# Performance work log

Hardware: AMD Instinct MI355X
Metric: run time of the kernel (lower is better)

Reference implementation:

```python
import jax, jax.numpy as jnp
import numpy as np

N = 100_000   # num destination nodes (adj rows)
M = 100_000   # num source/neighbor nodes (adj cols)
E = 3_200_000 # num edges (avg degree 32)
D_IN = 128
DIM = 128
LEAKY_ALPHA = 0.2  # tf.nn.leaky_relu default


def setup_inputs() -> dict:
    key = jax.random.key(0)
    ks = jax.random.split(key, 7)
    return {
        "self_embedding": jax.random.normal(ks[0], (N, D_IN), jnp.float32),
        "neigh_embedding": jax.random.normal(ks[1], (M, D_IN), jnp.float32),
        "W": jax.random.normal(ks[2], (D_IN, DIM), jnp.float32) / np.sqrt(D_IN).astype(np.float32),
        "w_self": jax.random.normal(ks[3], (DIM, 1), jnp.float32) * 0.1,
        "w_neigh": jax.random.normal(ks[4], (DIM, 1), jnp.float32) * 0.1,
        "edge_row": jax.random.randint(ks[5], (E,), 0, N, jnp.int32),
        "edge_col": jax.random.randint(ks[6], (E,), 0, M, jnp.int32),
    }


def reference(self_embedding, neigh_embedding, W, w_self, w_neigh, edge_row, edge_col):
    # Dense projections (shared weight, no bias)
    from_all = neigh_embedding @ W    # [M, DIM]
    from_self = self_embedding @ W    # [N, DIM]

    # Per-node attention logits
    self_weight = (from_self @ w_self)[:, 0]   # [N]
    all_weight = (from_all @ w_neigh)[:, 0]    # [M]

    # Per-edge score: leaky_relu(self_weight[row] + all_weight[col])
    scores = jax.nn.leaky_relu(self_weight[edge_row] + all_weight[edge_col],
                               negative_slope=LEAKY_ALPHA)  # [E]

    n = self_embedding.shape[0]
    # Sparse (segment) softmax over each row's edges, numerically stable
    row_max = jax.ops.segment_max(scores, edge_row, num_segments=n)
    row_max = jnp.where(jnp.isfinite(row_max), row_max, 0.0)  # guard empty rows
    e = jnp.exp(scores - row_max[edge_row])
    denom = jax.ops.segment_sum(e, edge_row, num_segments=n)
    denom = jnp.where(denom > 0, denom, 1.0)
    alpha = e / denom[edge_row]  # [E]

    # Sparse-dense matmul: output[i] = sum_j alpha_ij * from_all[j]
    agg = jax.ops.segment_sum(alpha[:, None] * from_all[edge_col], edge_row,
                              num_segments=n)  # [N, DIM]

    # renorm=False path: residual with from_self, then activation
    return jax.nn.relu(from_self + agg)
```

## Files before the change

kernel.cpp:

```cpp
#include <hip/hip_runtime.h>
#include <math.h>

#define DIM 128
#define LEAKY 0.2f
#define CAP 80
#define RPB 128
#define NBMAX 1024
#define PART_CHUNK 4096

typedef __attribute__((ext_vector_type(8))) short short8_t;
typedef __attribute__((ext_vector_type(8))) __bf16 bf16x8;
typedef __attribute__((ext_vector_type(4))) float f32x4;

__device__ __forceinline__ unsigned short f32_to_bf16_bits(float x) {
  unsigned u = __float_as_uint(x);
  u += 0x7fffu + ((u >> 16) & 1u);
  return (unsigned short)(u >> 16);
}

template <typename OT>
__global__ __launch_bounds__(256) void gemm_proj_mfma(
    const float* __restrict__ emb, const float* __restrict__ W,
    const float* __restrict__ wvec, OT* __restrict__ out,
    float* __restrict__ wout, int nrows)
{
  __shared__ unsigned short Wt[128 * 136];
  int t = threadIdx.x;
  int lane = t & 63;
  int wid = t >> 6;

  for (int i = t; i < 4096; i += 256) {
    int k = i >> 5;
    int c4 = (i & 31) << 2;
    float4 w4 = *(const float4*)(W + k * 128 + c4);
    Wt[(c4 + 0) * 136 + k] = f32_to_bf16_bits(w4.x);
    Wt[(c4 + 1) * 136 + k] = f32_to_bf16_bits(w4.y);
    Wt[(c4 + 2) * 136 + k] = f32_to_bf16_bits(w4.z);
    Wt[(c4 + 3) * 136 + k] = f32_to_bf16_bits(w4.w);
  }
  __syncthreads();

  int row0 = blockIdx.x * 128 + wid * 32;
  if (row0 >= nrows) return;

  int lr = lane & 15;
  int lk = lane >> 4;

  bf16x8 a[2][4];
#pragma unroll
  for (int rf = 0; rf < 2; rf++) {
    int row = row0 + rf * 16 + lr;
    row = min(row, nrows - 1);
    const float* src = emb + (size_t)row * DIM;
#pragma unroll
    for (int ks = 0; ks < 4; ks++) {
      int kb = ks * 32 + lk * 8;
      float4 x = *(const float4*)(src + kb);
      float4 y = *(const float4*)(src + kb + 4);
      union { short8_t s; bf16x8 b; } f;
      f.s[0] = (short)f32_to_bf16_bits(x.x); f.s[1] = (short)f32_to_bf16_bits(x.y);
      f.s[2] = (short)f32_to_bf16_bits(x.z); f.s[3] = (short)f32_to_bf16_bits(x.w);
      f.s[4] = (short)f32_to_bf16_bits(y.x); f.s[5] = (short)f32_to_bf16_bits(y.y);
      f.s[6] = (short)f32_to_bf16_bits(y.z); f.s[7] = (short)f32_to_bf16_bits(y.w);
      a[rf][ks] = f.b;
    }
  }

  f32x4 acc[2][8];
#pragma unroll
  for (int rf = 0; rf < 2; rf++)
#pragma unroll
    for (int cf = 0; cf < 8; cf++)
      acc[rf][cf] = (f32x4){0.f, 0.f, 0.f, 0.f};

#pragma unroll
  for (int ks = 0; ks < 4; ks++) {
#pragma unroll
    for (int cf = 0; cf < 8; cf++) {
      bf16x8 wf = *(const bf16x8*)(Wt + (cf * 16 + lr) * 136 + ks * 32 + lk * 8);
      acc[0][cf] = __builtin_amdgcn_mfma_f32_16x16x32_bf16(a[0][ks], wf, acc[0][cf], 0, 0, 0);
      acc[1][cf] = __builtin_amdgcn_mfma_f32_16x16x32_bf16(a[1][ks], wf, acc[1][cf], 0, 0, 0);
    }
  }

#pragma unroll
  for (int rf = 0; rf < 2; rf++) {
    float pp[4] = {0.f, 0.f, 0.f, 0.f};
#pragma unroll
    for (int cf = 0; cf < 8; cf++) {
      float wvv = wvec[cf * 16 + lr];
#pragma unroll
      for (int r = 0; r < 4; r++) pp[r] += acc[rf][cf][r] * wvv;
    }
#pragma unroll
    for (int r = 0; r < 4; r++) {
      pp[r] += __shfl_xor(pp[r], 1);
      pp[r] += __shfl_xor(pp[r], 2);
      pp[r] += __shfl_xor(pp[r], 4);
      pp[r] += __shfl_xor(pp[r], 8);
    }
#pragma unroll
    for (int r = 0; r < 4; r++) {
      int row = row0 + rf * 16 + lk * 4 + r;
      if (row < nrows) {
        if (lr == 0) wout[row] = pp[r];
#pragma unroll
        for (int cf = 0; cf < 8; cf++) {
          int col = cf * 16 + lr;
          if constexpr (sizeof(OT) == 4)
            ((float*)out)[(size_t)row * DIM + col] = acc[rf][cf][r];
          else
            ((unsigned short*)out)[(size_t)row * DIM + col] = f32_to_bf16_bits(acc[rf][cf][r]);
        }
      }
    }
  }
}

__global__ void zero_gcur(int* __restrict__ gcur, int nb)
{
  int i = blockIdx.x * blockDim.x + threadIdx.x;
  if (i < nb) gcur[i] = 0;
}

__global__ __launch_bounds__(256) void partition_edges(
    const int* __restrict__ erow, const int* __restrict__ ecol,
    unsigned* __restrict__ streams, int capB, int* __restrict__ gcur,
    int E, int nb)
{
  __shared__ int cnt[NBMAX];
  __shared__ int base_[NBMAX];
  __shared__ int pos[NBMAX];
  int t = threadIdx.x;
  for (int i = t; i < nb; i += 256) { cnt[i] = 0; pos[i] = 0; }
  __syncthreads();

  int e0 = blockIdx.x * PART_CHUNK + t * 16;
  int rows[16], cols[16];
#pragma unroll
  for (int q = 0; q < 4; q++) {
    int e = e0 + q * 4;
    if (e + 3 < E) {
      *(int4*)(rows + q * 4) = *(const int4*)(erow + e);
      *(int4*)(cols + q * 4) = *(const int4*)(ecol + e);
    } else {
#pragma unroll
      for (int j = 0; j < 4; j++) {
        rows[q * 4 + j] = (e + j < E) ? erow[e + j] : -1;
        cols[q * 4 + j] = (e + j < E) ? ecol[e + j] : 0;
      }
    }
  }
#pragma unroll
  for (int j = 0; j < 16; j++)
    if (rows[j] >= 0) atomicAdd(&cnt[rows[j] >> 7], 1);
  __syncthreads();
  for (int i = t; i < nb; i += 256)
    base_[i] = cnt[i] ? atomicAdd(gcur + i, cnt[i]) : 0;
  __syncthreads();
#pragma unroll
  for (int j = 0; j < 16; j++) {
    if (rows[j] >= 0) {
      int b = rows[j] >> 7;
      int idx = base_[b] + atomicAdd(&pos[b], 1);
      if (idx < capB)
        streams[(size_t)b * capB + idx] =
            (unsigned)cols[j] | ((unsigned)(rows[j] & (RPB - 1)) << 20);
    }
  }
}

__global__ __launch_bounds__(256) void bucket_scatter(
    const unsigned* __restrict__ streams, int capB,
    const int* __restrict__ gcur, int* __restrict__ perm,
    int* __restrict__ deg, int N)
{
  __shared__ __align__(16) unsigned slots[RPB * CAP];
  __shared__ int cnt[RPB];
  int b = blockIdx.x;
  int t = threadIdx.x;
  for (int i = t; i < RPB; i += 256) cnt[i] = 0;
  __syncthreads();

  int n = min(gcur[b], capB);
  const unsigned* s = streams + (size_t)b * capB;
  for (int i = t; i < n; i += 256) {
    unsigned v = s[i];
    int rl = v >> 20;
    int p = atomicAdd(&cnt[rl], 1);
    if (p < CAP) slots[rl * CAP + p] = v & 0xFFFFFu;
  }
  __syncthreads();

  int row0 = b * RPB;
  unsigned* dst = (unsigned*)(perm + (size_t)row0 * CAP);
  for (int i = t; i < RPB * CAP / 4; i += 256)
    *(uint4*)(dst + i * 4) = *(const uint4*)(slots + i * 4);
  for (int i = t; i < RPB; i += 256) {
    int row = row0 + i;
    if (row < N) deg[row] = min(cnt[i], CAP);
  }
}

__global__ __launch_bounds__(256) void aggregate_kernel(
    const unsigned short* __restrict__ from_all_bf16,
    const int* __restrict__ perm, const int* __restrict__ deg_arr,
    const float* __restrict__ sw, const float* __restrict__ aw,
    float* __restrict__ out, int n)
{
  int wid = threadIdx.x >> 6;
  int lane = threadIdx.x & 63;
  int row = blockIdx.x * 4 + wid;
  if (row >= n) return;
  int deg = deg_arr[row];
  size_t base = (size_t)row * CAP;

  int g  = lane >> 4;
  int sl = lane & 15;

  size_t o = (size_t)row * DIM + sl * 8;
  float4 r0, r1;
  if (g == 0) {
    r0 = *(const float4*)(out + o);
    r1 = *(const float4*)(out + o + 4);
  }

  float acc[8];
#pragma unroll
  for (int k = 0; k < 8; k++) acc[k] = 0.f;
  float dsum = 0.f;
  float swr = sw[row];

  for (int bb = 0; bb < deg; bb += 64) {
    int nact = min(64, deg - bb);
    int c = 0; float e = 0.f;
    if (lane < nact) {
      c = perm[base + bb + lane];
      float v = swr + aw[c];
      v = v > 0.f ? v : LEAKY * v;
      e = __expf(v);
    }
    dsum += e;

    for (int half = 0; half < 2; half++) {
      if (half * 32 >= nact) break;
#pragma unroll
      for (int jj = 0; jj < 8; jj++) {
        int eidx = half * 32 + (jj << 2) + g;
        int   cj = __shfl(c, eidx);
        float ej = __shfl(e, eidx);
        uint4 u = *(const uint4*)(from_all_bf16 + (size_t)cj * DIM + sl * 8);
        acc[0] += ej * __uint_as_float(u.x << 16);
        acc[1] += ej * __uint_as_float(u.x & 0xffff0000u);
        acc[2] += ej * __uint_as_float(u.y << 16);
        acc[3] += ej * __uint_as_float(u.y & 0xffff0000u);
        acc[4] += ej * __uint_as_float(u.z << 16);
        acc[5] += ej * __uint_as_float(u.z & 0xffff0000u);
        acc[6] += ej * __uint_as_float(u.w << 16);
        acc[7] += ej * __uint_as_float(u.w & 0xffff0000u);
      }
    }
  }

#pragma unroll
  for (int off = 32; off >= 1; off >>= 1) dsum += __shfl_xor(dsum, off);
#pragma unroll
  for (int k = 0; k < 8; k++) {
    acc[k] += __shfl_xor(acc[k], 16);
    acc[k] += __shfl_xor(acc[k], 32);
  }
  float inv = dsum > 0.f ? 1.f / dsum : 1.f;

  if (g == 0) {
    r0.x += acc[0] * inv; r0.y += acc[1] * inv;
    r0.z += acc[2] * inv; r0.w += acc[3] * inv;
    r1.x += acc[4] * inv; r1.y += acc[5] * inv;
    r1.z += acc[6] * inv; r1.w += acc[7] * inv;
    r0.x = r0.x > 0.f ? r0.x : 0.f; r0.y = r0.y > 0.f ? r0.y : 0.f;
    r0.z = r0.z > 0.f ? r0.z : 0.f; r0.w = r0.w > 0.f ? r0.w : 0.f;
    r1.x = r1.x > 0.f ? r1.x : 0.f; r1.y = r1.y > 0.f ? r1.y : 0.f;
    r1.z = r1.z > 0.f ? r1.z : 0.f; r1.w = r1.w > 0.f ? r1.w : 0.f;
    *(float4*)(out + o) = r0;
    *(float4*)(out + o + 4) = r1;
  }
}

extern "C" void kernel_launch(void* const* d_in, const int* in_sizes, int n_in,
                              void* d_out, int out_size, void* d_ws, size_t ws_size,
                              hipStream_t stream)
{
  const float* self_emb  = (const float*)d_in[0];
  const float* neigh_emb = (const float*)d_in[1];
  const float* W         = (const float*)d_in[2];
  const float* w_self    = (const float*)d_in[3];
  const float* w_neigh   = (const float*)d_in[4];
  const int*   erow      = (const int*)d_in[5];
  const int*   ecol      = (const int*)d_in[6];

  const int N = in_sizes[0] / DIM;
  const int M = in_sizes[1] / DIM;
  const int E = in_sizes[5];

  float* out = (float*)d_out;

  char* ws = (char*)d_ws;
  size_t off = 0;
  auto alloc = [&](size_t bytes) -> char* {
    char* p = ws + off;
    off += (bytes + 255) & ~(size_t)255;
    return p;
  };
  unsigned short* from_all = (unsigned short*)alloc((size_t)M * DIM * sizeof(unsigned short));
  float* all_w   = (float*)alloc((size_t)M * sizeof(float));
  float* self_w  = (float*)alloc((size_t)N * sizeof(float));
  int*   deg     = (int*)alloc((size_t)N * sizeof(int));
  int*   gcur    = (int*)alloc(NBMAX * sizeof(int));
  int*   perm    = (int*)alloc((size_t)N * CAP * sizeof(int));

  const int nb = (N + RPB - 1) / RPB;
  const int capB = E / nb + 1024;
  unsigned* streams = (unsigned*)alloc((size_t)nb * capB * sizeof(unsigned));

  gemm_proj_mfma<unsigned short><<<(M + 127) / 128, 256, 0, stream>>>(neigh_emb, W, w_neigh, from_all, all_w, M);
  gemm_proj_mfma<float><<<(N + 127) / 128, 256, 0, stream>>>(self_emb, W, w_self, out, self_w, N);

  zero_gcur<<<(nb + 255) / 256, 256, 0, stream>>>(gcur, nb);

  int pblocks = (E + PART_CHUNK - 1) / PART_CHUNK;
  partition_edges<<<pblocks, 256, 0, stream>>>(erow, ecol, streams, capB, gcur, E, nb);

  bucket_scatter<<<nb, 256, 0, stream>>>(streams, capB, gcur, perm, deg, N);

  aggregate_kernel<<<(N + 3) / 4, 256, 0, stream>>>(from_all, perm, deg,
                                                    self_w, all_w, out, N);
}
```

Before: 245.5 us.

## Sort row neighbors by column region, persistent aggregate grid, trimmed perm writes

Bucket scatter now stages each bucket's edge stream in shared memory and does a two-pass counting sort. Within each row, neighbor columns are grouped by column region (col >> 13), so gathers of from_all rows in aggregation have better L2 locality. Perm writes skip chunks past each row's degree. Partitioning reads edges twice in larger chunks instead of holding 16 per thread in registers. Aggregation uses a fixed 2048-block grid-stride loop. The extra sort pass and the larger shared-memory footprint may reduce occupancy in bucket_scatter.

```diff
diff --git a/kernel.cpp b/kernel.cpp
--- a/kernel.cpp
+++ b/kernel.cpp
@@ -6,7 +6,10 @@
 #define CAP 80
 #define RPB 128
 #define NBMAX 1024
-#define PART_CHUNK 4096
+#define PART_CHUNK 8192
+#define STAGE_MAX 5120
+#define RSH 13
+#define NREG_MAX 16
 
 typedef __attribute__((ext_vector_type(8))) short short8_t;
 typedef __attribute__((ext_vector_type(8))) __bf16 bf16x8;
@@ -135,153 +138,189 @@
   for (int i = t; i < nb; i += 256) { cnt[i] = 0; pos[i] = 0; }
   __syncthreads();
 
-  int e0 = blockIdx.x * PART_CHUNK + t * 16;
-  int rows[16], cols[16];
-#pragma unroll
-  for (int q = 0; q < 4; q++) {
-    int e = e0 + q * 4;
-    if (e + 3 < E) {
-      *(int4*)(rows + q * 4) = *(const int4*)(erow + e);
-      *(int4*)(cols + q * 4) = *(const int4*)(ecol + e);
+  int e0 = blockIdx.x * PART_CHUNK;
+  int e1 = min(E, e0 + PART_CHUNK);
+
+  for (int i = e0 + t * 4; i < e1; i += 1024) {
+    if (i + 3 < e1) {
+      int4 r = *(const int4*)(erow + i);
+      atomicAdd(&cnt[r.x >> 7], 1); atomicAdd(&cnt[r.y >> 7], 1);
+      atomicAdd(&cnt[r.z >> 7], 1); atomicAdd(&cnt[r.w >> 7], 1);
     } else {
-#pragma unroll
-      for (int j = 0; j < 4; j++) {
-        rows[q * 4 + j] = (e + j < E) ? erow[e + j] : -1;
-        cols[q * 4 + j] = (e + j < E) ? ecol[e + j] : 0;
-      }
-    }
-  }
-#pragma unroll
-  for (int j = 0; j < 16; j++)
-    if (rows[j] >= 0) atomicAdd(&cnt[rows[j] >> 7], 1);
+      for (int j = 0; j < e1 - i; j++) atomicAdd(&cnt[erow[i + j] >> 7], 1);
+    }
+  }
   __syncthreads();
   for (int i = t; i < nb; i += 256)
     base_[i] = cnt[i] ? atomicAdd(gcur + i, cnt[i]) : 0;
   __syncthreads();
-#pragma unroll
-  for (int j = 0; j < 16; j++) {
-    if (rows[j] >= 0) {
-      int b = rows[j] >> 7;
-      int idx = base_[b] + atomicAdd(&pos[b], 1);
-      if (idx < capB)
-        streams[(size_t)b * capB + idx] =
-            (unsigned)cols[j] | ((unsigned)(rows[j] & (RPB - 1)) << 20);
-    }
-  }
-}
-
-__global__ __launch_bounds__(256) void bucket_scatter(
+  for (int i = e0 + t * 4; i < e1; i += 1024) {
+    int nv = min(4, e1 - i);
+    if (nv == 4) {
+      int4 r = *(const int4*)(erow + i);
+      int4 c = *(const int4*)(ecol + i);
+      int rr[4] = {r.x, r.y, r.z, r.w};
+      int cc[4] = {c.x, c.y, c.z, c.w};
+#pragma unroll
+      for (int j = 0; j < 4; j++) {
+        int b = rr[j] >> 7;
+        int idx = base_[b] + atomicAdd(&pos[b], 1);
+        if (idx < capB)
+          streams[(size_t)b * capB + idx] =
+              (unsigned)cc[j] | ((unsigned)(rr[j] & (RPB - 1)) << 20);
+      }
+    } else {
+      for (int j = 0; j < nv; j++) {
+        int row = erow[i + j], col = ecol[i + j];
+        int b = row >> 7;
+        int idx = base_[b] + atomicAdd(&pos[b], 1);
+        if (idx < capB)
+          streams[(size_t)b * capB + idx] =
+              (unsigned)col | ((unsigned)(row & (RPB - 1)) << 20);
+      }
+    }
+  }
+}
+
+__global__ __launch_bounds__(256, 2) void bucket_scatter(
     const unsigned* __restrict__ streams, int capB,
-    const int* __restrict__ gcur, int* __restrict__ perm,
-    int* __restrict__ deg, int N)
+    const int* __restrict__ gcur, unsigned* __restrict__ perm,
+    int* __restrict__ deg, int N, int nreg)
 {
   __shared__ __align__(16) unsigned slots[RPB * CAP];
-  __shared__ int cnt[RPB];
+  __shared__ unsigned stage[STAGE_MAX];
+  __shared__ int cnt[RPB][NREG_MAX];
+  __shared__ int start_[RPB][NREG_MAX];
+  __shared__ int rowdeg[RPB];
+
   int b = blockIdx.x;
   int t = threadIdx.x;
-  for (int i = t; i < RPB; i += 256) cnt[i] = 0;
-  __syncthreads();
-
   int n = min(gcur[b], capB);
   const unsigned* s = streams + (size_t)b * capB;
+
+  for (int i = t; i < RPB * NREG_MAX; i += 256) ((int*)cnt)[i] = 0;
+  for (int i = t; i < n; i += 256) stage[i] = s[i];
+  __syncthreads();
+
   for (int i = t; i < n; i += 256) {
-    unsigned v = s[i];
+    unsigned v = stage[i];
+    atomicAdd(&cnt[v >> 20][(v & 0xFFFFFu) >> RSH], 1);
+  }
+  __syncthreads();
+
+  if (t < RPB) {
+    int run = 0;
+    for (int r = 0; r < nreg; r++) {
+      start_[t][r] = run;
+      run += cnt[t][r];
+      cnt[t][r] = 0;
+    }
+    rowdeg[t] = min(run, CAP);
+    int row = b * RPB + t;
+    if (row < N) deg[row] = min(run, CAP);
+  }
+  __syncthreads();
+
+  for (int i = t; i < n; i += 256) {
+    unsigned v = stage[i];
     int rl = v >> 20;
-    int p = atomicAdd(&cnt[rl], 1);
-    if (p < CAP) slots[rl * CAP + p] = v & 0xFFFFFu;
+    unsigned col = v & 0xFFFFFu;
+    int reg = col >> RSH;
+    int p = start_[rl][reg] + atomicAdd(&cnt[rl][reg], 1);
+    if (p < CAP) slots[rl * CAP + p] = col;
   }
   __syncthreads();
 
   int row0 = b * RPB;
-  unsigned* dst = (unsigned*)(perm + (size_t)row0 * CAP);
-  for (int i = t; i < RPB * CAP / 4; i += 256)
-    *(uint4*)(dst + i * 4) = *(const uint4*)(slots + i * 4);
-  for (int i = t; i < RPB; i += 256) {
-    int row = row0 + i;
-    if (row < N) deg[row] = min(cnt[i], CAP);
+  unsigned* dst = perm + (size_t)row0 * CAP;
+  const int W4 = CAP / 4;
+  for (int i = t; i < RPB * W4; i += 256) {
+    int rl = i / W4, w = i - rl * W4;
+    if (w * 4 < rowdeg[rl])
+      *(uint4*)(dst + rl * CAP + w * 4) = *(const uint4*)(slots + rl * CAP + w * 4);
   }
 }
 
 __global__ __launch_bounds__(256) void aggregate_kernel(
     const unsigned short* __restrict__ from_all_bf16,
-    const int* __restrict__ perm, const int* __restrict__ deg_arr,
+    const unsigned* __restrict__ perm, const int* __restrict__ deg_arr,
     const float* __restrict__ sw, const float* __restrict__ aw,
-    float* __restrict__ out, int n)
+    float* __restrict__ out, int n, int rstride)
 {
   int wid = threadIdx.x >> 6;
   int lane = threadIdx.x & 63;
-  int row = blockIdx.x * 4 + wid;
-  if (row >= n) return;
-  int deg = deg_arr[row];
-  size_t base = (size_t)row * CAP;
-
   int g  = lane >> 4;
   int sl = lane & 15;
 
-  size_t o = (size_t)row * DIM + sl * 8;
-  float4 r0, r1;
-  if (g == 0) {
-    r0 = *(const float4*)(out + o);
-    r1 = *(const float4*)(out + o + 4);
-  }
-
-  float acc[8];
-#pragma unroll
-  for (int k = 0; k < 8; k++) acc[k] = 0.f;
-  float dsum = 0.f;
-  float swr = sw[row];
-
-  for (int bb = 0; bb < deg; bb += 64) {
-    int nact = min(64, deg - bb);
-    int c = 0; float e = 0.f;
-    if (lane < nact) {
-      c = perm[base + bb + lane];
-      float v = swr + aw[c];
-      v = v > 0.f ? v : LEAKY * v;
-      e = __expf(v);
-    }
-    dsum += e;
-
-    for (int half = 0; half < 2; half++) {
-      if (half * 32 >= nact) break;
-#pragma unroll
-      for (int jj = 0; jj < 8; jj++) {
-        int eidx = half * 32 + (jj << 2) + g;
-        int   cj = __shfl(c, eidx);
-        float ej = __shfl(e, eidx);
-        uint4 u = *(const uint4*)(from_all_bf16 + (size_t)cj * DIM + sl * 8);
-        acc[0] += ej * __uint_as_float(u.x << 16);
-        acc[1] += ej * __uint_as_float(u.x & 0xffff0000u);
-        acc[2] += ej * __uint_as_float(u.y << 16);
-        acc[3] += ej * __uint_as_float(u.y & 0xffff0000u);
-        acc[4] += ej * __uint_as_float(u.z << 16);
-        acc[5] += ej * __uint_as_float(u.z & 0xffff0000u);
-        acc[6] += ej * __uint_as_float(u.w << 16);
-        acc[7] += ej * __uint_as_float(u.w & 0xffff0000u);
-      }
-    }
-  }
-
-#pragma unroll
-  for (int off = 32; off >= 1; off >>= 1) dsum += __shfl_xor(dsum, off);
-#pragma unroll
-  for (int k = 0; k < 8; k++) {
-    acc[k] += __shfl_xor(acc[k], 16);
-    acc[k] += __shfl_xor(acc[k], 32);
-  }
-  float inv = dsum > 0.f ? 1.f / dsum : 1.f;
-
-  if (g == 0) {
-    r0.x += acc[0] * inv; r0.y += acc[1] * inv;
-    r0.z += acc[2] * inv; r0.w += acc[3] * inv;
-    r1.x += acc[4] * inv; r1.y += acc[5] * inv;
-    r1.z += acc[6] * inv; r1.w += acc[7] * inv;
-    r0.x = r0.x > 0.f ? r0.x : 0.f; r0.y = r0.y > 0.f ? r0.y : 0.f;
-    r0.z = r0.z > 0.f ? r0.z : 0.f; r0.w = r0.w > 0.f ? r0.w : 0.f;
-    r1.x = r1.x > 0.f ? r1.x : 0.f; r1.y = r1.y > 0.f ? r1.y : 0.f;
-    r1.z = r1.z > 0.f ? r1.z : 0.f; r1.w = r1.w > 0.f ? r1.w : 0.f;
-    *(float4*)(out + o) = r0;
-    *(float4*)(out + o + 4) = r1;
+  for (int row = blockIdx.x * 4 + wid; row < n; row += rstride) {
+    int deg = deg_arr[row];
+    size_t base = (size_t)row * CAP;
+
+    size_t o = (size_t)row * DIM + sl * 8;
+    float4 r0, r1;
+    if (g == 0) {
+      r0 = *(const float4*)(out + o);
+      r1 = *(const float4*)(out + o + 4);
+    }
+
+    float acc[8];
+#pragma unroll
+    for (int k = 0; k < 8; k++) acc[k] = 0.f;
+    float dsum = 0.f;
+    float swr = sw[row];
+
+    for (int bb = 0; bb < deg; bb += 64) {
+      int nact = min(64, deg - bb);
+      int c = 0; float e = 0.f;
+      if (lane < nact) {
+        c = (int)perm[base + bb + lane];
+        float v = swr + aw[c];
+        v = v > 0.f ? v : LEAKY * v;
+        e = __expf(v);
+      }
+      dsum += e;
+
+      for (int half = 0; half < 2; half++) {
+        if (half * 32 >= nact) break;
+#pragma unroll
+        for (int jj = 0; jj < 8; jj++) {
+          int eidx = half * 32 + (jj << 2) + g;
+          int   cj = __shfl(c, eidx);
+          float ej = __shfl(e, eidx);
+          uint4 u = *(const uint4*)(from_all_bf16 + (size_t)cj * DIM + sl * 8);
+          acc[0] += ej * __uint_as_float(u.x << 16);
+          acc[1] += ej * __uint_as_float(u.x & 0xffff0000u);
+          acc[2] += ej * __uint_as_float(u.y << 16);
+          acc[3] += ej * __uint_as_float(u.y & 0xffff0000u);
+          acc[4] += ej * __uint_as_float(u.z << 16);
+          acc[5] += ej * __uint_as_float(u.z & 0xffff0000u);
+          acc[6] += ej * __uint_as_float(u.w << 16);
+          acc[7] += ej * __uint_as_float(u.w & 0xffff0000u);
+        }
+      }
+    }
+
+#pragma unroll
+    for (int off = 32; off >= 1; off >>= 1) dsum += __shfl_xor(dsum, off);
+#pragma unroll
+    for (int k = 0; k < 8; k++) {
+      acc[k] += __shfl_xor(acc[k], 16);
+      acc[k] += __shfl_xor(acc[k], 32);
+    }
+    float inv = dsum > 0.f ? 1.f / dsum : 1.f;
+
+    if (g == 0) {
+      r0.x += acc[0] * inv; r0.y += acc[1] * inv;
+      r0.z += acc[2] * inv; r0.w += acc[3] * inv;
+      r1.x += acc[4] * inv; r1.y += acc[5] * inv;
+      r1.z += acc[6] * inv; r1.w += acc[7] * inv;
+      r0.x = r0.x > 0.f ? r0.x : 0.f; r0.y = r0.y > 0.f ? r0.y : 0.f;
+      r0.z = r0.z > 0.f ? r0.z : 0.f; r0.w = r0.w > 0.f ? r0.w : 0.f;
+      r1.x = r1.x > 0.f ? r1.x : 0.f; r1.y = r1.y > 0.f ? r1.y : 0.f;
+      r1.z = r1.z > 0.f ? r1.z : 0.f; r1.w = r1.w > 0.f ? r1.w : 0.f;
+      *(float4*)(out + o) = r0;
+      *(float4*)(out + o + 4) = r1;
+    }
   }
 }
 
@@ -315,11 +354,14 @@
   float* self_w  = (float*)alloc((size_t)N * sizeof(float));
   int*   deg     = (int*)alloc((size_t)N * sizeof(int));
   int*   gcur    = (int*)alloc(NBMAX * sizeof(int));
-  int*   perm    = (int*)alloc((size_t)N * CAP * sizeof(int));
+  unsigned* perm = (unsigned*)alloc((size_t)N * CAP * sizeof(unsigned));
 
   const int nb = (N + RPB - 1) / RPB;
-  const int capB = E / nb + 1024;
+  int capB = E / nb + 1024;
+  if (capB > STAGE_MAX) capB = STAGE_MAX;
   unsigned* streams = (unsigned*)alloc((size_t)nb * capB * sizeof(unsigned));
+
+  const int nreg = ((M - 1) >> RSH) + 1;
 
   gemm_proj_mfma<unsigned short><<<(M + 127) / 128, 256, 0, stream>>>(neigh_emb, W, w_neigh, from_all, all_w, M);
   gemm_proj_mfma<float><<<(N + 127) / 128, 256, 0, stream>>>(self_emb, W, w_self, out, self_w, N);
@@ -329,8 +371,9 @@
   int pblocks = (E + PART_CHUNK - 1) / PART_CHUNK;
   partition_edges<<<pblocks, 256, 0, stream>>>(erow, ecol, streams, capB, gcur, E, nb);
 
-  bucket_scatter<<<nb, 256, 0, stream>>>(streams, capB, gcur, perm, deg, N);
-
-  aggregate_kernel<<<(N + 3) / 4, 256, 0, stream>>>(from_all, perm, deg,
-                                                    self_w, all_w, out, N);
-}
+  bucket_scatter<<<nb, 256, 0, stream>>>(streams, capB, gcur, perm, deg, N, nreg);
+
+  const int ablocks = 2048;
+  aggregate_kernel<<<ablocks, 256, 0, stream>>>(from_all, perm, deg,
+                                                self_w, all_w, out, N, ablocks * 4);
+}
```

Result: slower. 253.0 us (+3.1%).

## Quantize neighbor projections to per-row int8 for the gather-aggregate

Applied to the files above, without the earlier changes.

Adds a pass that quantizes the bf16 neighbor projection rows to offset uint8 with a per-row scale. The aggregation kernel then gathers 128-byte rows instead of 256-byte rows and processes 8 edges per wave iteration with 16 channels per lane. The 128 offset is corrected through a summed weight term. This halves the gather traffic of the memory-bound aggregation but adds quantization error beyond bf16, plus an extra kernel and workspace.

```diff
diff --git a/kernel.cpp b/kernel.cpp
--- a/kernel.cpp
+++ b/kernel.cpp
@@ -117,6 +117,28 @@
   }
 }
 
+__global__ __launch_bounds__(256) void quantize_rows(
+    const unsigned short* __restrict__ fa_bf16,
+    unsigned char* __restrict__ fa_i8, float* __restrict__ scales, int M)
+{
+  int wid = threadIdx.x >> 6;
+  int lane = threadIdx.x & 63;
+  int row = blockIdx.x * 4 + wid;
+  if (row >= M) return;
+  unsigned u = ((const unsigned*)(fa_bf16 + (size_t)row * DIM))[lane];
+  float v0 = __uint_as_float(u << 16);
+  float v1 = __uint_as_float(u & 0xffff0000u);
+  float m = fmaxf(fabsf(v0), fabsf(v1));
+#pragma unroll
+  for (int off = 32; off >= 1; off >>= 1) m = fmaxf(m, __shfl_xor(m, off));
+  float inv = m > 0.f ? 127.f / m : 0.f;
+  int q0 = (int)__builtin_rintf(v0 * inv) + 128;
+  int q1 = (int)__builtin_rintf(v1 * inv) + 128;
+  ((unsigned short*)(fa_i8 + (size_t)row * DIM))[lane] =
+      (unsigned short)((q0 & 0xff) | ((q1 & 0xff) << 8));
+  if (lane == 0) scales[row] = m * (1.f / 127.f);
+}
+
 __global__ void zero_gcur(int* __restrict__ gcur, int nb)
 {
   int i = blockIdx.x * blockDim.x + threadIdx.x;
@@ -203,7 +225,8 @@
 }
 
 __global__ __launch_bounds__(256) void aggregate_kernel(
-    const unsigned short* __restrict__ from_all_bf16,
+    const unsigned char* __restrict__ fa_i8,
+    const float* __restrict__ scales,
     const int* __restrict__ perm, const int* __restrict__ deg_arr,
     const float* __restrict__ sw, const float* __restrict__ aw,
     float* __restrict__ out, int n)
@@ -215,73 +238,89 @@
   int deg = deg_arr[row];
   size_t base = (size_t)row * CAP;
 
-  int g  = lane >> 4;
-  int sl = lane & 15;
-
-  size_t o = (size_t)row * DIM + sl * 8;
-  float4 r0, r1;
+  int g  = lane >> 3;
+  int sl = lane & 7;
+
+  size_t o = (size_t)row * DIM + sl * 16;
+  float4 rr0, rr1, rr2, rr3;
   if (g == 0) {
-    r0 = *(const float4*)(out + o);
-    r1 = *(const float4*)(out + o + 4);
-  }
-
-  float acc[8];
-#pragma unroll
-  for (int k = 0; k < 8; k++) acc[k] = 0.f;
-  float dsum = 0.f;
+    rr0 = *(const float4*)(out + o);
+    rr1 = *(const float4*)(out + o + 4);
+    rr2 = *(const float4*)(out + o + 8);
+    rr3 = *(const float4*)(out + o + 12);
+  }
+
+  float acc[16];
+#pragma unroll
+  for (int k = 0; k < 16; k++) acc[k] = 0.f;
+  float dsum = 0.f, Bl = 0.f;
   float swr = sw[row];
 
   for (int bb = 0; bb < deg; bb += 64) {
     int nact = min(64, deg - bb);
-    int c = 0; float e = 0.f;
+    int c = 0; float e = 0.f, a = 0.f;
     if (lane < nact) {
       c = perm[base + bb + lane];
       float v = swr + aw[c];
       v = v > 0.f ? v : LEAKY * v;
       e = __expf(v);
+      a = e * scales[c];
     }
     dsum += e;
 
     for (int half = 0; half < 2; half++) {
       if (half * 32 >= nact) break;
 #pragma unroll
-      for (int jj = 0; jj < 8; jj++) {
-        int eidx = half * 32 + (jj << 2) + g;
+      for (int jj = 0; jj < 4; jj++) {
+        int eidx = half * 32 + (jj << 3) + g;
+        float aj = __shfl(a, eidx);
         int   cj = __shfl(c, eidx);
-        float ej = __shfl(e, eidx);
-        uint4 u = *(const uint4*)(from_all_bf16 + (size_t)cj * DIM + sl * 8);
-        acc[0] += ej * __uint_as_float(u.x << 16);
-        acc[1] += ej * __uint_as_float(u.x & 0xffff0000u);
-        acc[2] += ej * __uint_as_float(u.y << 16);
-        acc[3] += ej * __uint_as_float(u.y & 0xffff0000u);
-        acc[4] += ej * __uint_as_float(u.z << 16);
-        acc[5] += ej * __uint_as_float(u.z & 0xffff0000u);
-        acc[6] += ej * __uint_as_float(u.w << 16);
-        acc[7] += ej * __uint_as_float(u.w & 0xffff0000u);
+        uint4 u = *(const uint4*)(fa_i8 + (size_t)cj * DIM + sl * 16);
+        Bl += aj;
+        acc[0]  += aj * (float)( u.x        & 0xffu);
+        acc[1]  += aj * (float)((u.x >> 8 ) & 0xffu);
+        acc[2]  += aj * (float)((u.x >> 16) & 0xffu);
+        acc[3]  += aj * (float)( u.x >> 24);
+        acc[4]  += aj * (float)( u.y        & 0xffu);
+        acc[5]  += aj * (float)((u.y >> 8 ) & 0xffu);
+        acc[6]  += aj * (float)((u.y >> 16) & 0xffu);
+        acc[7]  += aj * (float)( u.y >> 24);
+        acc[8]  += aj * (float)( u.z        & 0xffu);
+        acc[9]  += aj * (float)((u.z >> 8 ) & 0xffu);
+        acc[10] += aj * (float)((u.z >> 16) & 0xffu);
+        acc[11] += aj * (float)( u.z >> 24);
+        acc[12] += aj * (float)( u.w        & 0xffu);
+        acc[13] += aj * (float)((u.w >> 8 ) & 0xffu);
+        acc[14] += aj * (float)((u.w >> 16) & 0xffu);
+        acc[15] += aj * (float)( u.w >> 24);
       }
     }
   }
 
 #pragma unroll
   for (int off = 32; off >= 1; off >>= 1) dsum += __shfl_xor(dsum, off);
-#pragma unroll
-  for (int k = 0; k < 8; k++) {
+  Bl += __shfl_xor(Bl, 8); Bl += __shfl_xor(Bl, 16); Bl += __shfl_xor(Bl, 32);
+#pragma unroll
+  for (int k = 0; k < 16; k++) {
+    acc[k] += __shfl_xor(acc[k], 8);
     acc[k] += __shfl_xor(acc[k], 16);
     acc[k] += __shfl_xor(acc[k], 32);
   }
+  float B = -128.f * Bl;
   float inv = dsum > 0.f ? 1.f / dsum : 1.f;
 
   if (g == 0) {
-    r0.x += acc[0] * inv; r0.y += acc[1] * inv;
-    r0.z += acc[2] * inv; r0.w += acc[3] * inv;
-    r1.x += acc[4] * inv; r1.y += acc[5] * inv;
-    r1.z += acc[6] * inv; r1.w += acc[7] * inv;
-    r0.x = r0.x > 0.f ? r0.x : 0.f; r0.y = r0.y > 0.f ? r0.y : 0.f;
-    r0.z = r0.z > 0.f ? r0.z : 0.f; r0.w = r0.w > 0.f ? r0.w : 0.f;
-    r1.x = r1.x > 0.f ? r1.x : 0.f; r1.y = r1.y > 0.f ? r1.y : 0.f;
-    r1.z = r1.z > 0.f ? r1.z : 0.f; r1.w = r1.w > 0.f ? r1.w : 0.f;
-    *(float4*)(out + o) = r0;
-    *(float4*)(out + o + 4) = r1;
+    float r[16] = {rr0.x, rr0.y, rr0.z, rr0.w, rr1.x, rr1.y, rr1.z, rr1.w,
+                   rr2.x, rr2.y, rr2.z, rr2.w, rr3.x, rr3.y, rr3.z, rr3.w};
+#pragma unroll
+    for (int k = 0; k < 16; k++) {
+      float x = r[k] + (acc[k] + B) * inv;
+      r[k] = x > 0.f ? x : 0.f;
+    }
+    *(float4*)(out + o)      = make_float4(r[0],  r[1],  r[2],  r[3]);
+    *(float4*)(out + o + 4)  = make_float4(r[4],  r[5],  r[6],  r[7]);
+    *(float4*)(out + o + 8)  = make_float4(r[8],  r[9],  r[10], r[11]);
+    *(float4*)(out + o + 12) = make_float4(r[12], r[13], r[14], r[15]);
   }
 }
 
@@ -311,6 +350,8 @@
     return p;
   };
   unsigned short* from_all = (unsigned short*)alloc((size_t)M * DIM * sizeof(unsigned short));
+  unsigned char*  fa_i8    = (unsigned char*)alloc((size_t)M * DIM);
+  float* scales  = (float*)alloc((size_t)M * sizeof(float));
   float* all_w   = (float*)alloc((size_t)M * sizeof(float));
   float* self_w  = (float*)alloc((size_t)N * sizeof(float));
   int*   deg     = (int*)alloc((size_t)N * sizeof(int));
@@ -322,6 +363,7 @@
   unsigned* streams = (unsigned*)alloc((size_t)nb * capB * sizeof(unsigned));
 
   gemm_proj_mfma<unsigned short><<<(M + 127) / 128, 256, 0, stream>>>(neigh_emb, W, w_neigh, from_all, all_w, M);
+  quantize_rows<<<(M + 3) / 4, 256, 0, stream>>>(from_all, fa_i8, scales, M);
   gemm_proj_mfma<float><<<(N + 127) / 128, 256, 0, stream>>>(self_emb, W, w_self, out, self_w, N);
 
   zero_gcur<<<(nb + 255) / 256, 256, 0, stream>>>(gcur, nb);
@@ -331,6 +373,6 @@
 
   bucket_scatter<<<nb, 256, 0, stream>>>(streams, capB, gcur, perm, deg, N);
 
-  aggregate_kernel<<<(N + 3) / 4, 256, 0, stream>>>(from_all, perm, deg,
+  aggregate_kernel<<<(N + 3) / 4, 256, 0, stream>>>(fa_i8, scales, perm, deg,
                                                     self_w, all_w, out, N);
 }
```

Measured after the change: 250.5 us. +2.0%, slower.
